# Performance work log

Measured on AMD Instinct MI355X. Metric: run time of the kernel, lower is better.

## Reference

```python
import jax, jax.numpy as jnp
import numpy as np

N = 50000   # nodes
E = 400000  # edges (before self-loops)
F = 128     # num_features
H = 8       # heads (layer 1)
C = 64      # hidden_channels
B = 64      # graphs in batch
K = 10      # num_classes
NEG_SLOPE = 0.2


def setup_inputs() -> dict:
    key = jax.random.key(0)
    ks = jax.random.split(key, 12)
    g = lambda k, shape, fan: jax.random.normal(k, shape, jnp.float32) / np.sqrt(fan).astype(np.float32)
    return {
        "x": jax.random.normal(ks[0], (N, F), jnp.float32),
        "edge_index": jax.random.randint(ks[1], (2, E), 0, N, jnp.int32),
        "batch": jnp.sort(jax.random.randint(ks[2], (N,), 0, B, jnp.int32)),
        "W1": g(ks[3], (F, H * C), F),
        "att_src1": g(ks[4], (H, C), C),
        "att_dst1": g(ks[5], (H, C), C),
        "b1": jnp.zeros((H * C,), jnp.float32),
        "W2": g(ks[6], (H * C, C), H * C),
        "att_src2": g(ks[7], (1, C), C),
        "att_dst2": g(ks[8], (1, C), C),
        "b2": jnp.zeros((C,), jnp.float32),
        "lin1_w": g(ks[9], (C, C), C),
        "lin1_b": jnp.zeros((C,), jnp.float32),
        "lin2_w": g(ks[10], (C, K), C),
        "lin2_b": jnp.zeros((K,), jnp.float32),
    }


def gat_conv(x, src, dst, W, att_src, att_dst, bias):
    """PyG GATConv (self-loops already appended to src/dst). x:[N,Fin] -> [N,H*C]."""
    heads, out_c = att_src.shape
    h = (x @ W).reshape(N, heads, out_c)                      # [N,H,C]
    a_s = jnp.einsum('nhc,hc->nh', h, att_src)                # [N,H]
    a_d = jnp.einsum('nhc,hc->nh', h, att_dst)
    e = jax.nn.leaky_relu(a_s[src] + a_d[dst], NEG_SLOPE)     # [E',H]
    # segment softmax over incoming edges of each destination node
    m = jax.ops.segment_max(e, dst, num_segments=N)
    e = jnp.exp(e - m[dst])
    denom = jax.ops.segment_sum(e, dst, num_segments=N)
    alpha = e / (denom[dst] + 1e-16)                          # [E',H]
    out = jax.ops.segment_sum(h[src] * alpha[:, :, None], dst, num_segments=N)  # [N,H,C]
    return out.reshape(N, heads * out_c) + bias


def reference(x, edge_index, batch, W1, att_src1, att_dst1, b1,
              W2, att_src2, att_dst2, b2, lin1_w, lin1_b, lin2_w, lin2_b):
    loops = jnp.arange(N, dtype=edge_index.dtype)
    src = jnp.concatenate([edge_index[0], loops])
    dst = jnp.concatenate([edge_index[1], loops])

    h = gat_conv(x, src, dst, W1, att_src1, att_dst1, b1)     # [N, H*C]
    h = jax.nn.elu(h)                                         # dropout inactive (eval)
    h = gat_conv(h, src, dst, W2, att_src2, att_dst2, b2)     # [N, C]
    h = jax.nn.elu(h)

    pooled = jax.ops.segment_sum(h, batch, num_segments=B)    # global_add_pool -> [B, C]
    z = jax.nn.elu(pooled @ lin1_w + lin1_b)
    logits = z @ lin2_w + lin2_b
    return jax.nn.log_softmax(logits, axis=-1)
```

## Files before the change

### kernel.cpp

```cpp
#include <hip/hip_runtime.h>
#include <hip/hip_bf16.h>

#define DEV static __device__ __forceinline__

constexpr int F1 = 128;
constexpr int H1 = 8;
constexpr int C  = 64;
constexpr int B  = 64;
constexpr int K  = 10;
constexpr float NEG = 0.2f;

typedef __attribute__((ext_vector_type(8))) short short8;
typedef __attribute__((ext_vector_type(4))) float floatx4;

DEV float b2f(__hip_bfloat16 x) { return __bfloat162float(x); }
DEV float elu1(float v) { return v > 0.f ? v : (__expf(v) - 1.f); }
DEV unsigned short f2bbits(float f) {
  __hip_bfloat16 b = __float2bfloat16(f);
  return *(unsigned short*)&b;
}
DEV float blo(unsigned u) { return __uint_as_float(u << 16); }
DEV float bhi(unsigned u) { return __uint_as_float(u & 0xffff0000u); }
DEV float bu(unsigned short u) { return __uint_as_float(((unsigned)u) << 16); }
DEV unsigned pack2(float lo, float hi) {
  return (unsigned)f2bbits(lo) | ((unsigned)f2bbits(hi) << 16);
}


DEV int detect_dev(const void* xraw, int* lds) {
  if (threadIdx.x == 0) {
    const __hip_bfloat16* xb = (const __hip_bfloat16*)xraw;
    int bad = 0;
    for (int i = 0; i < 128; ++i) {
      float v = b2f(xb[2 * i]);
      if (!(fabsf(v) < 1e4f)) bad++;
    }
    *lds = (bad < 13) ? 1 : 0;
  }
  __syncthreads();
  return *lds;
}

#define CVT(p, i) (isbf ? b2f(((const __hip_bfloat16*)(p))[i]) : ((const float*)(p))[i])

__global__ void fused_prep_kernel(const void* x_raw, const void* w1raw,
                                  const void* as1r, const void* ad1r, const void* b1r,
                                  const void* w2raw,
                                  const void* as2r, const void* ad2r, const void* b2r,
                                  const void* l1wr, const void* l1br,
                                  const void* l2wr, const void* l2br,
                                  unsigned short* __restrict__ xbf,
                                  unsigned short* __restrict__ w1frag,
                                  unsigned short* __restrict__ w2frag,
                                  float* __restrict__ wts,
                                  int* __restrict__ deg,
                                  float* __restrict__ pooled,
                                  int nX, int N) {
  __shared__ int fl;
  int isbf = detect_dev(x_raw, &fl);
  int gid = blockIdx.x * 256 + threadIdx.x;
  int stride = gridDim.x * 256;

  if (isbf) {
    const unsigned short* src = (const unsigned short*)x_raw;
    for (int i = gid; i < nX; i += stride) xbf[i] = src[i];
  } else {
    const float* src = (const float*)x_raw;
    for (int i = gid; i < nX; i += stride) xbf[i] = f2bbits(src[i]);
  }
  for (int i = gid; i < 512;  i += stride) wts[0    + i] = CVT(as1r, i);
  for (int i = gid; i < 512;  i += stride) wts[512  + i] = CVT(ad1r, i);
  for (int i = gid; i < 512;  i += stride) {
    int hp = i >> 7, l16 = (i >> 3) & 15, nt = i & 7;
    int c = hp * 128 + nt * 16 + l16;
    wts[1024 + i] = CVT(b1r, c);
  }
  for (int i = gid; i < 64;   i += stride) wts[1536 + i] = CVT(as2r, i);
  for (int i = gid; i < 64;   i += stride) wts[1600 + i] = CVT(ad2r, i);
  for (int i = gid; i < 64;   i += stride) wts[1664 + i] = CVT(b2r, i);
  for (int i = gid; i < 4096; i += stride) wts[1728 + i] = CVT(l1wr, i);
  for (int i = gid; i < 64;   i += stride) wts[5824 + i] = CVT(l1br, i);
  for (int i = gid; i < 640;  i += stride) wts[5888 + i] = CVT(l2wr, i);
  for (int i = gid; i < 10;   i += stride) wts[6528 + i] = CVT(l2br, i);
  for (int t = gid; t < 8192; t += stride) {
    int lane = t & 63, ks = (t >> 6) & 3, nt = t >> 8;
    for (int j = 0; j < 8; ++j) {
      int k = ks * 32 + (lane >> 4) * 8 + j;
      int n = nt * 16 + (lane & 15);
      w1frag[t * 8 + j] = f2bbits(CVT(w1raw, k * 512 + n));
    }
  }
  for (int t = gid; t < 4096; t += stride) {
    int lane = t & 63, nt = (t >> 6) & 3, ks = t >> 8;
    for (int j = 0; j < 8; ++j) {
      int p = ks * 32 + (lane >> 4) * 8 + j;
      int hp = p >> 7, pl16 = (p >> 3) & 15, pnt = p & 7;
      int k = hp * 128 + pnt * 16 + pl16;
      int n = nt * 16 + (lane & 15);
      w2frag[t * 8 + j] = f2bbits(CVT(w2raw, k * 64 + n));
    }
  }
  for (int i = gid; i < N; i += stride) deg[i] = 0;
  for (int i = gid; i < B * C; i += stride) pooled[i] = 0.f;
}

__global__ void deg_count_kernel(const int* __restrict__ ei, int E, int Etot,
                                 int* __restrict__ deg) {
  int e = blockIdx.x * blockDim.x + threadIdx.x;
  if (e >= Etot) return;
  int d = (e < E) ? ei[E + e] : e - E;
  atomicAdd(&deg[d], 1);
}

__global__ void scan_block_kernel(const int* __restrict__ deg,
                                  int* __restrict__ local,
                                  int* __restrict__ bsum, int N) {
  __shared__ int tmp[256];
  int t = threadIdx.x;
  int i = blockIdx.x * 256 + t;
  int v = (i < N) ? deg[i] : 0;
  tmp[t] = v;
  __syncthreads();
  for (int off = 1; off < 256; off <<= 1) {
    int u = (t >= off) ? tmp[t - off] : 0;
    __syncthreads();
    tmp[t] += u;
    __syncthreads();
  }
  if (i < N) local[i] = tmp[t] - v;
  if (t == 255) bsum[blockIdx.x] = tmp[255];
}

__global__ void scan_finish_kernel(const int* __restrict__ local,
                                   const int* __restrict__ bsum, int nb,
                                   int* __restrict__ rowptr,
                                   int* __restrict__ cursor, int N, int Etot) {
  __shared__ int tmp[256];
  __shared__ int offs;
  int t = threadIdx.x;
  int v0 = (t < nb) ? bsum[t] : 0;
  tmp[t] = v0;
  __syncthreads();
  for (int off = 1; off < 256; off <<= 1) {
    int u = (t >= off) ? tmp[t - off] : 0;
    __syncthreads();
    tmp[t] += u;
    __syncthreads();
  }
  if (t == (int)blockIdx.x) offs = tmp[t] - v0;
  __syncthreads();
  int i = blockIdx.x * 256 + t;
  if (i < N) {
    int r = local[i] + offs;
    rowptr[i] = r;
    cursor[i] = r;
  }
  if (i == 0) rowptr[N] = Etot;
}

__global__ __launch_bounds__(256) void gemm1_att_kernel(
    const unsigned short* __restrict__ xbf,
    const unsigned short* __restrict__ W1frag,
    const float* __restrict__ att_src,
    const float* __restrict__ att_dst,
    float* __restrict__ a_s, float* __restrict__ a_d,
    int N) {
  __shared__ __align__(16) unsigned short Xls[64 * 136];
  int t = threadIdx.x;
  int w = t >> 6, lane = t & 63;
  int quad = lane >> 4, l16 = lane & 15;
  int blkbase = blockIdx.x * 64;
  int rowbase = blkbase + w * 16;

  for (int idx = t; idx < 1024; idx += 256) {
    int row = idx >> 4, c = idx & 15;
    int rg = blkbase + row; if (rg >= N) rg = N - 1;
    *(uint4*)&Xls[row * 136 + c * 8] =
        *(const uint4*)(xbf + (size_t)rg * 128 + c * 8);
  }
  __syncthreads();

  short8 afr[4];
  {
    int rl = w * 16 + l16;
#pragma unroll
    for (int ks = 0; ks < 4; ++ks)
      afr[ks] = *(const short8*)&Xls[rl * 136 + ks * 32 + quad * 8];
  }

  for (int hp = 0; hp < 4; ++hp) {
    floatx4 acc[8] = {};
    const unsigned short* Bp = W1frag + (size_t)hp * 16384;
#pragma unroll
    for (int nt = 0; nt < 8; ++nt)
#pragma unroll
      for (int ks = 0; ks < 4; ++ks) {
        short8 b = *(const short8*)&Bp[((nt * 4 + ks) * 64 + lane) * 8];
        acc[nt] = __builtin_amdgcn_mfma_f32_16x16x32_bf16(afr[ks], b, acc[nt], 0, 0, 0);
      }

    float asw[8], adw[8];
#pragma unroll
    for (int nt = 0; nt < 8; ++nt) {
      asw[nt] = att_src[hp * 128 + nt * 16 + l16];
      adw[nt] = att_dst[hp * 128 + nt * 16 + l16];
    }
    float ps[2][4] = {}, pd[2][4] = {};
#pragma unroll
    for (int nt = 0; nt < 8; ++nt) {
      int hl = nt >> 2;
#pragma unroll
      for (int r = 0; r < 4; ++r) {
        ps[hl][r] += acc[nt][r] * asw[nt];
        pd[hl][r] += acc[nt][r] * adw[nt];
      }
    }
#pragma unroll
    for (int hl = 0; hl < 2; ++hl)
#pragma unroll
      for (int r = 0; r < 4; ++r) {
        float p = ps[hl][r], q = pd[hl][r];
#pragma unroll
        for (int off = 1; off < 16; off <<= 1) {
          p += __shfl_xor(p, off);
          q += __shfl_xor(q, off);
        }
        int row = rowbase + quad * 4 + r;
        if (l16 == 0 && row < N) {
          a_s[(size_t)row * 8 + hp * 2 + hl] = p;
          a_d[(size_t)row * 8 + hp * 2 + hl] = q;
        }
      }
  }
}

__global__ void fill_weight_kernel(const int* __restrict__ ei, int E, int Etot,
                                   const float* __restrict__ a_s,
                                   const float* __restrict__ a_d,
                                   int* __restrict__ cursor,
                                   int* __restrict__ col,
                                   float* __restrict__ wedge) {
  int e = blockIdx.x * 256 + threadIdx.x;
  if (e >= Etot) return;
  int s, d;
  if (e < E) { s = ei[e]; d = ei[E + e]; } else { s = d = e - E; }
  int pos = atomicAdd(&cursor[d], 1);
  col[pos] = s;
  float4 s0 = *(const float4*)(a_s + (size_t)s * 8);
  float4 s1 = *(const float4*)(a_s + (size_t)s * 8 + 4);
  float4 d0 = *(const float4*)(a_d + (size_t)d * 8);
  float4 d1 = *(const float4*)(a_d + (size_t)d * 8 + 4);
  float4 w0, w1;
  float v;
  v = s0.x + d0.x; v = v > 0.f ? v : NEG * v; w0.x = __expf(v);
  v = s0.y + d0.y; v = v > 0.f ? v : NEG * v; w0.y = __expf(v);
  v = s0.z + d0.z; v = v > 0.f ? v : NEG * v; w0.z = __expf(v);
  v = s0.w + d0.w; v = v > 0.f ? v : NEG * v; w0.w = __expf(v);
  v = s1.x + d1.x; v = v > 0.f ? v : NEG * v; w1.x = __expf(v);
  v = s1.y + d1.y; v = v > 0.f ? v : NEG * v; w1.y = __expf(v);
  v = s1.z + d1.z; v = v > 0.f ? v : NEG * v; w1.z = __expf(v);
  v = s1.w + d1.w; v = v > 0.f ? v : NEG * v; w1.w = __expf(v);
  *(float4*)(wedge + (size_t)pos * 8)     = w0;
  *(float4*)(wedge + (size_t)pos * 8 + 4) = w1;
}

__global__ __launch_bounds__(256) void aggx_gemm1_kernel(
    const unsigned short* __restrict__ xbf,
    const unsigned short* __restrict__ W1frag,
    const int* __restrict__ rowptr,
    const int* __restrict__ col,
    const float* __restrict__ wedge,
    const float* __restrict__ bias_perm,
    unsigned short* __restrict__ out1,
    int N) {
  __shared__ __align__(16) unsigned short Agg[8 * 16 * 136];
  int t = threadIdx.x, w = t >> 6, lane = t & 63;
  int dbase = blockIdx.x * 16;
  const unsigned* xd = (const unsigned*)xbf;
  unsigned* AggU = (unsigned*)Agg;

  for (int j = 0; j < 4; ++j) {
    int dloc = w * 4 + j;
    int d = dbase + dloc;
    int dd = d < N ? d : N - 1;
    int beg = rowptr[dd], end = rowptr[dd + 1];
    float acc[16] = {};
    float dn[8] = {};
#pragma unroll 4
    for (int i = beg; i < end; ++i) {
      int iu = __builtin_amdgcn_readfirstlane(i);
      int s = col[iu];
      unsigned xv = xd[(size_t)s * 64 + lane];
      float4 wa = *(const float4*)(wedge + (size_t)iu * 8);
      float4 wb = *(const float4*)(wedge + (size_t)iu * 8 + 4);
      float x0 = blo(xv), x1 = bhi(xv);
      acc[0]  += wa.x * x0; acc[1]  += wa.x * x1; dn[0] += wa.x;
      acc[2]  += wa.y * x0; acc[3]  += wa.y * x1; dn[1] += wa.y;
      acc[4]  += wa.z * x0; acc[5]  += wa.z * x1; dn[2] += wa.z;
      acc[6]  += wa.w * x0; acc[7]  += wa.w * x1; dn[3] += wa.w;
      acc[8]  += wb.x * x0; acc[9]  += wb.x * x1; dn[4] += wb.x;
      acc[10] += wb.y * x0; acc[11] += wb.y * x1; dn[5] += wb.y;
      acc[12] += wb.z * x0; acc[13] += wb.z * x1; dn[6] += wb.z;
      acc[14] += wb.w * x0; acc[15] += wb.w * x1; dn[7] += wb.w;
    }
#pragma unroll
    for (int h = 0; h < 8; ++h) {
      float inv = 1.f / (dn[h] + 1e-16f);
      AggU[(h * 16 + dloc) * 68 + lane] =
          pack2(acc[2 * h] * inv, acc[2 * h + 1] * inv);
    }
  }
  __syncthreads();

  int quad = lane >> 4, l16 = lane & 15;
  int hp = w;
  short8 afr[2][4];
#pragma unroll
  for (int hh = 0; hh < 2; ++hh) {
    int h = hp * 2 + hh;
#pragma unroll
    for (int ks = 0; ks < 4; ++ks)
      afr[hh][ks] = *(const short8*)&Agg[(h * 16 + l16) * 136 + ks * 32 + quad * 8];
  }
  floatx4 acc2[8] = {};
  const unsigned short* Bp = W1frag + (size_t)hp * 16384;
#pragma unroll
  for (int nt = 0; nt < 8; ++nt) {
    int hh = nt >> 2;
#pragma unroll
    for (int ks = 0; ks < 4; ++ks) {
      short8 b = *(const short8*)&Bp[((nt * 4 + ks) * 64 + lane) * 8];
      acc2[nt] = __builtin_amdgcn_mfma_f32_16x16x32_bf16(afr[hh][ks], b, acc2[nt], 0, 0, 0);
    }
  }
  float4 b0 = *(const float4*)&bias_perm[hp * 128 + l16 * 8];
  float4 b1 = *(const float4*)&bias_perm[hp * 128 + l16 * 8 + 4];
#pragma unroll
  for (int r = 0; r < 4; ++r) {
    int row = dbase + quad * 4 + r;
    if (row < N) {
      uint4 o;
      o.x = pack2(elu1(acc2[0][r] + b0.x), elu1(acc2[1][r] + b0.y));
      o.y = pack2(elu1(acc2[2][r] + b0.z), elu1(acc2[3][r] + b0.w));
      o.z = pack2(elu1(acc2[4][r] + b1.x), elu1(acc2[5][r] + b1.y));
      o.w = pack2(elu1(acc2[6][r] + b1.z), elu1(acc2[7][r] + b1.w));
      *(uint4*)&out1[(size_t)row * 512 + hp * 128 + l16 * 8] = o;
    }
  }
}

__global__ __launch_bounds__(256) void gemm2_mfma_kernel(
    const unsigned short* __restrict__ x2bf,
    const unsigned short* __restrict__ W2frag,
    const float* __restrict__ att_src,
    const float* __restrict__ att_dst,
    unsigned short* __restrict__ h2,
    float* __restrict__ a_s, float* __restrict__ a_d,
    int N) {
  int t = threadIdx.x;
  int w = t >> 6, lane = t & 63;
  int quad = lane >> 4, l16 = lane & 15;
  int rowbase = blockIdx.x * 64 + w * 16;

  floatx4 acc[4] = {};
  int r0 = rowbase + l16; if (r0 >= N) r0 = N - 1;
  const unsigned short* p0 = x2bf + (size_t)r0 * 512 + quad * 8;
#pragma unroll
  for (int ks = 0; ks < 16; ++ks) {
    short8 a0 = *(const short8*)(p0 + ks * 32);
#pragma unroll
    for (int nt = 0; nt < 4; ++nt) {
      short8 b = *(const short8*)&W2frag[((ks * 4 + nt) * 64 + lane) * 8];
      acc[nt] = __builtin_amdgcn_mfma_f32_16x16x32_bf16(a0, b, acc[nt], 0, 0, 0);
    }
  }

  float asw[4], adw[4];
#pragma unroll
  for (int nt = 0; nt < 4; ++nt) {
    asw[nt] = att_src[nt * 16 + l16];
    adw[nt] = att_dst[nt * 16 + l16];
  }
  float ps[4] = {}, pd[4] = {};
#pragma unroll
  for (int nt = 0; nt < 4; ++nt)
#pragma unroll
    for (int r = 0; r < 4; ++r) {
      float v = acc[nt][r];
      int row = rowbase + quad * 4 + r;
      if (row < N) h2[(size_t)row * 64 + nt * 16 + l16] = f2bbits(v);
      ps[r] += v * asw[nt];
      pd[r] += v * adw[nt];
    }
#pragma unroll
  for (int r = 0; r < 4; ++r) {
    float p = ps[r], q = pd[r];
#pragma unroll
    for (int off = 1; off < 16; off <<= 1) {
      p += __shfl_xor(p, off);
      q += __shfl_xor(q, off);
    }
    int row = rowbase + quad * 4 + r;
    if (l16 == 0 && row < N) {
      a_s[row] = p;
      a_d[row] = q;
    }
  }
}

__global__ void gat_agg1_kernel(const int* __restrict__ rowptr,
                                const int* __restrict__ col,
                                const float* __restrict__ a_s,
                                const float* __restrict__ a_d,
                                const unsigned short* __restrict__ hfeat,
                                const float* __restrict__ bias,
                                unsigned short* __restrict__ out, int N) {
  int wave = threadIdx.x >> 6, lane = threadIdx.x & 63;
  int d = blockIdx.x * 4 + wave;
  if (d >= N) return;
  int beg = rowptr[d], end = rowptr[d + 1];
  int qg = lane >> 4, l16 = lane & 15;
  float adv = a_d[d];
  const uint2* hfu = (const uint2*)hfeat;
  float acc[4] = {};
  float wsum = 0.f;
#pragma unroll 2
  for (int i = beg + qg; i < end; i += 4) {
    int s = col[i];
    float v = a_s[s] + adv;
    v = v > 0.f ? v : NEG * v;
    float wv = __expf(v);
    wsum += wv;
    uint2 u = hfu[(size_t)s * 16 + l16];
    acc[0] += wv * blo(u.x); acc[1] += wv * bhi(u.x);
    acc[2] += wv * blo(u.y); acc[3] += wv * bhi(u.y);
  }
#pragma unroll
  for (int off = 16; off <= 32; off <<= 1) {
#pragma unroll
    for (int j = 0; j < 4; ++j) acc[j] += __shfl_xor(acc[j], off);
    wsum += __shfl_xor(wsum, off);
  }
  float winv = 1.f / (wsum + 1e-16f);
  float4 bb = ((const float4*)bias)[l16];
  float r0 = elu1(acc[0] * winv + bb.x), r1 = elu1(acc[1] * winv + bb.y);
  float r2 = elu1(acc[2] * winv + bb.z), r3 = elu1(acc[3] * winv + bb.w);
  if (qg == 0) {
    uint2 o; o.x = pack2(r0, r1); o.y = pack2(r2, r3);
    ((uint2*)out)[(size_t)d * 16 + l16] = o;
  }
}

__global__ void pool_kernel(const unsigned short* __restrict__ out2,
                            const int* __restrict__ batch,
                            float* __restrict__ pooled, int N) {
  int wave = threadIdx.x >> 6, lane = threadIdx.x & 63;
  int seg = blockIdx.x * 4 + wave;
  int start = seg * 16;
  if (start >= N) return;
  int end = min(start + 16, N);
  int cur = batch[start];
  float acc = 0.f;
  for (int n = start; n < end; ++n) {
    int bn = batch[n];
    if (bn != cur) {
      unsafeAtomicAdd(&pooled[cur * 64 + lane], acc);
      acc = 0.f; cur = bn;
    }
    acc += bu(out2[(size_t)n * 64 + lane]);
  }
  unsafeAtomicAdd(&pooled[cur * 64 + lane], acc);
}

__global__ void head_kernel(const float* __restrict__ pooled,
                            const float* __restrict__ lin1_w,
                            const float* __restrict__ lin1_b,
                            const float* __restrict__ lin2_w,
                            const float* __restrict__ lin2_b,
                            const void* __restrict__ x_raw,
                            void* __restrict__ outv) {
  __shared__ float P[C];
  __shared__ float Zs[C];
  __shared__ float Ls[K];
  __shared__ float lse_s;
  __shared__ int fl;
  int isbf = detect_dev(x_raw, &fl);
  int g = blockIdx.x, t = threadIdx.x;
  P[t] = pooled[g * C + t];
  __syncthreads();
  float acc = lin1_b[t];
  for (int k = 0; k < C; ++k) acc += P[k] * lin1_w[k * C + t];
  Zs[t] = elu1(acc);
  __syncthreads();
  if (t < K) {
    float a = lin2_b[t];
    for (int k = 0; k < C; ++k) a += Zs[k] * lin2_w[k * K + t];
    Ls[t] = a;
  }
  __syncthreads();
  if (t == 0) {
    float mx = -1e30f;
    for (int c = 0; c < K; ++c) mx = fmaxf(mx, Ls[c]);
    float s = 0.f;
    for (int c = 0; c < K; ++c) s += __expf(Ls[c] - mx);
    lse_s = mx + __logf(s);
  }
  __syncthreads();
  if (t < K) {
    float val = Ls[t] - lse_s;
    if (isbf) ((__hip_bfloat16*)outv)[g * K + t] = __float2bfloat16(val);
    else      ((float*)outv)[g * K + t] = val;
  }
}

extern "C" void kernel_launch(void* const* d_in, const int* in_sizes, int n_in,
                              void* d_out, int out_size, void* d_ws, size_t ws_size,
                              hipStream_t stream) {
  const void* x_raw = d_in[0];
  const int*  ei    = (const int*)d_in[1];
  const int*  batch = (const int*)d_in[2];

  const int N    = in_sizes[2];
  const int E    = in_sizes[1] / 2;
  const int Etot = E + N;
  const int nb   = (N + 255) / 256;

  float* ws   = (float*)d_ws;
  size_t off  = 0;

  float* wts = ws + off; off += 6544;
  float* as1w = wts + 0;
  float* ad1w = wts + 512;
  float* b1w  = wts + 1024;
  float* as2w = wts + 1536;
  float* ad2w = wts + 1600;
  float* b2w  = wts + 1664;
  float* l1w  = wts + 1728;
  float* l1b  = wts + 5824;
  float* l2w  = wts + 5888;
  float* l2b  = wts + 6528;

  unsigned short* xbf    = (unsigned short*)(ws + off); off += (size_t)N * 64;
  unsigned short* w1frag = (unsigned short*)(ws + off); off += 32768;
  unsigned short* w2frag = (unsigned short*)(ws + off); off += 16384;
  float* wedge           = ws + off;                    off += (size_t)Etot * 8;
  unsigned short* out1bf = (unsigned short*)(ws + off); off += (size_t)N * 256;
  unsigned short* h2bf   = (unsigned short*)(ws + off); off += (size_t)N * 32;
  unsigned short* out2bf = (unsigned short*)(ws + off); off += (size_t)N * 32;
  float* as1  = ws + off; off += (size_t)N * H1;
  float* ad1  = ws + off; off += (size_t)N * H1;
  float* as2  = ws + off; off += (size_t)N;
  float* ad2  = ws + off; off += (size_t)N;
  float* pooled = ws + off; off += (size_t)B * C;

  int* ibase  = (int*)(ws + off);
  int* deg    = ibase;                 ibase += N;
  int* cursor = ibase;                 ibase += N;
  int* rowptr = ibase;                 ibase += N + 1;
  int* locals = ibase;                 ibase += N;
  int* bsum   = ibase;                 ibase += 256;
  int* col    = ibase;                 ibase += Etot;

  fused_prep_kernel<<<1024, 256, 0, stream>>>(
      x_raw, d_in[3], d_in[4], d_in[5], d_in[6], d_in[7], d_in[8], d_in[9],
      d_in[10], d_in[11], d_in[12], d_in[13], d_in[14],
      xbf, w1frag, w2frag, wts, deg, pooled, in_sizes[0], N);

  deg_count_kernel<<<(Etot + 255) / 256, 256, 0, stream>>>(ei, E, Etot, deg);
  scan_block_kernel<<<nb, 256, 0, stream>>>(deg, locals, bsum, N);
  scan_finish_kernel<<<nb, 256, 0, stream>>>(locals, bsum, nb, rowptr, cursor, N, Etot);

  gemm1_att_kernel<<<(N + 63) / 64, 256, 0, stream>>>(xbf, w1frag, as1w, ad1w,
                                                      as1, ad1, N);

  fill_weight_kernel<<<(Etot + 255) / 256, 256, 0, stream>>>(
      ei, E, Etot, as1, ad1, cursor, col, wedge);

  aggx_gemm1_kernel<<<(N + 15) / 16, 256, 0, stream>>>(
      xbf, w1frag, rowptr, col, wedge, b1w, out1bf, N);

  gemm2_mfma_kernel<<<(N + 63) / 64, 256, 0, stream>>>(out1bf, w2frag, as2w, ad2w,
                                                       h2bf, as2, ad2, N);
  gat_agg1_kernel<<<(N + 3) / 4, 256, 0, stream>>>(rowptr, col, as2, ad2, h2bf, b2w, out2bf, N);

  pool_kernel<<<(N + 63) / 64, 256, 0, stream>>>(out2bf, batch, pooled, N);
  head_kernel<<<B, 64, 0, stream>>>(pooled, l1w, l1b, l2w, l2b, x_raw, (void*)d_out);
}
```

Baseline: 332.0 us.

## Fold attention vectors into W1 and restructure layer-1 aggregation blocks

Precomputes W1·att_src and W1·att_dst into a small 128x16 bf16 MFMA fragment, so layer-1 attention scalars come from a single K=128 MFMA per row tile instead of a full 128x512 GEMM followed by reductions. The aggregation+GEMM kernel moves to 512 threads with 8 destinations per block, one warp per destination, and uses packed v_pk_fma/v_pk_add with SGPR-broadcast weights plus an approximate reciprocal refined by one Newton step. This removes a large redundant GEMM. The trade-offs are a different rounding order for the attention scalars (the folded vector is rounded to bf16) and half-filled 16-row MFMA tiles in the aggregation kernel.

Result: faster. 303.8 us (-8.5%).

```diff
diff --git a/kernel.cpp b/kernel.cpp
--- a/kernel.cpp
+++ b/kernel.cpp
@@ -12,6 +12,7 @@
 
 typedef __attribute__((ext_vector_type(8))) short short8;
 typedef __attribute__((ext_vector_type(4))) float floatx4;
+typedef __attribute__((ext_vector_type(2))) float floatx2;
 
 DEV float b2f(__hip_bfloat16 x) { return __bfloat162float(x); }
 DEV float elu1(float v) { return v > 0.f ? v : (__expf(v) - 1.f); }
@@ -24,6 +25,16 @@
 DEV float bu(unsigned short u) { return __uint_as_float(((unsigned)u) << 16); }
 DEV unsigned pack2(float lo, float hi) {
   return (unsigned)f2bbits(lo) | ((unsigned)f2bbits(hi) << 16);
+}
+DEV float rcp_nr(float x) {
+  float r = __builtin_amdgcn_rcpf(x);
+  return r * (2.f - x * r);
+}
+DEV void pk_fma(floatx2& acc, floatx2 x, floatx2 w) {
+  asm("v_pk_fma_f32 %0, %1, %2, %0" : "+v"(acc) : "v"(x), "s"(w));
+}
+DEV void pk_add(floatx2& acc, floatx2 w) {
+  asm("v_pk_add_f32 %0, %0, %1" : "+v"(acc) : "s"(w));
 }
 
 
@@ -52,6 +63,7 @@
                                   unsigned short* __restrict__ xbf,
                                   unsigned short* __restrict__ w1frag,
                                   unsigned short* __restrict__ w2frag,
+                                  unsigned short* __restrict__ vfrag,
                                   float* __restrict__ wts,
                                   int* __restrict__ deg,
                                   float* __restrict__ pooled,
@@ -68,8 +80,6 @@
     const float* src = (const float*)x_raw;
     for (int i = gid; i < nX; i += stride) xbf[i] = f2bbits(src[i]);
   }
-  for (int i = gid; i < 512;  i += stride) wts[0    + i] = CVT(as1r, i);
-  for (int i = gid; i < 512;  i += stride) wts[512  + i] = CVT(ad1r, i);
   for (int i = gid; i < 512;  i += stride) {
     int hp = i >> 7, l16 = (i >> 3) & 15, nt = i & 7;
     int c = hp * 128 + nt * 16 + l16;
@@ -100,6 +110,21 @@
       w2frag[t * 8 + j] = f2bbits(CVT(w2raw, k * 64 + n));
     }
   }
+  for (int t = gid; t < 2048; t += stride) {
+    int j = t & 7, lane = (t >> 3) & 63, ks = t >> 9;
+    int k = ks * 32 + (lane >> 4) * 8 + j;
+    int n = lane & 15;
+    int hh = (n < 8) ? n : (n - 8);
+    float s = 0.f;
+    if (n < 8) {
+      for (int c = 0; c < 64; ++c)
+        s += CVT(w1raw, k * 512 + hh * 64 + c) * CVT(as1r, hh * 64 + c);
+    } else {
+      for (int c = 0; c < 64; ++c)
+        s += CVT(w1raw, k * 512 + hh * 64 + c) * CVT(ad1r, hh * 64 + c);
+    }
+    vfrag[(ks * 64 + lane) * 8 + j] = f2bbits(s);
+  }
   for (int i = gid; i < N; i += stride) deg[i] = 0;
   for (int i = gid; i < B * C; i += stride) pooled[i] = 0.f;
 }
@@ -158,79 +183,31 @@
   if (i == 0) rowptr[N] = Etot;
 }
 
-__global__ __launch_bounds__(256) void gemm1_att_kernel(
+__global__ __launch_bounds__(256) void att_scalars_kernel(
     const unsigned short* __restrict__ xbf,
-    const unsigned short* __restrict__ W1frag,
-    const float* __restrict__ att_src,
-    const float* __restrict__ att_dst,
+    const unsigned short* __restrict__ vfrag,
     float* __restrict__ a_s, float* __restrict__ a_d,
     int N) {
-  __shared__ __align__(16) unsigned short Xls[64 * 136];
-  int t = threadIdx.x;
-  int w = t >> 6, lane = t & 63;
+  int t = threadIdx.x, w = t >> 6, lane = t & 63;
   int quad = lane >> 4, l16 = lane & 15;
-  int blkbase = blockIdx.x * 64;
-  int rowbase = blkbase + w * 16;
-
-  for (int idx = t; idx < 1024; idx += 256) {
-    int row = idx >> 4, c = idx & 15;
-    int rg = blkbase + row; if (rg >= N) rg = N - 1;
-    *(uint4*)&Xls[row * 136 + c * 8] =
-        *(const uint4*)(xbf + (size_t)rg * 128 + c * 8);
-  }
-  __syncthreads();
-
-  short8 afr[4];
-  {
-    int rl = w * 16 + l16;
-#pragma unroll
-    for (int ks = 0; ks < 4; ++ks)
-      afr[ks] = *(const short8*)&Xls[rl * 136 + ks * 32 + quad * 8];
-  }
-
-  for (int hp = 0; hp < 4; ++hp) {
-    floatx4 acc[8] = {};
-    const unsigned short* Bp = W1frag + (size_t)hp * 16384;
-#pragma unroll
-    for (int nt = 0; nt < 8; ++nt)
-#pragma unroll
-      for (int ks = 0; ks < 4; ++ks) {
-        short8 b = *(const short8*)&Bp[((nt * 4 + ks) * 64 + lane) * 8];
-        acc[nt] = __builtin_amdgcn_mfma_f32_16x16x32_bf16(afr[ks], b, acc[nt], 0, 0, 0);
-      }
-
-    float asw[8], adw[8];
-#pragma unroll
-    for (int nt = 0; nt < 8; ++nt) {
-      asw[nt] = att_src[hp * 128 + nt * 16 + l16];
-      adw[nt] = att_dst[hp * 128 + nt * 16 + l16];
-    }
-    float ps[2][4] = {}, pd[2][4] = {};
-#pragma unroll
-    for (int nt = 0; nt < 8; ++nt) {
-      int hl = nt >> 2;
-#pragma unroll
-      for (int r = 0; r < 4; ++r) {
-        ps[hl][r] += acc[nt][r] * asw[nt];
-        pd[hl][r] += acc[nt][r] * adw[nt];
-      }
-    }
-#pragma unroll
-    for (int hl = 0; hl < 2; ++hl)
-#pragma unroll
-      for (int r = 0; r < 4; ++r) {
-        float p = ps[hl][r], q = pd[hl][r];
-#pragma unroll
-        for (int off = 1; off < 16; off <<= 1) {
-          p += __shfl_xor(p, off);
-          q += __shfl_xor(q, off);
-        }
-        int row = rowbase + quad * 4 + r;
-        if (l16 == 0 && row < N) {
-          a_s[(size_t)row * 8 + hp * 2 + hl] = p;
-          a_d[(size_t)row * 8 + hp * 2 + hl] = q;
-        }
-      }
+  int row0 = blockIdx.x * 64 + w * 16;
+
+  floatx4 acc = {};
+  int rl = row0 + l16; if (rl >= N) rl = N - 1;
+  const unsigned short* xp = xbf + (size_t)rl * 128 + quad * 8;
+#pragma unroll
+  for (int ks = 0; ks < 4; ++ks) {
+    short8 a = *(const short8*)(xp + ks * 32);
+    short8 b = *(const short8*)&vfrag[(ks * 64 + lane) * 8];
+    acc = __builtin_amdgcn_mfma_f32_16x16x32_bf16(a, b, acc, 0, 0, 0);
+  }
+#pragma unroll
+  for (int r = 0; r < 4; ++r) {
+    int row = row0 + quad * 4 + r;
+    if (row < N) {
+      if (l16 < 8) a_s[(size_t)row * 8 + l16] = acc[r];
+      else         a_d[(size_t)row * 8 + (l16 - 8)] = acc[r];
+    }
   }
 }
 
@@ -264,7 +241,7 @@
   *(float4*)(wedge + (size_t)pos * 8 + 4) = w1;
 }
 
-__global__ __launch_bounds__(256) void aggx_gemm1_kernel(
+__global__ __launch_bounds__(512, 8) void aggx_gemm1_kernel(
     const unsigned short* __restrict__ xbf,
     const unsigned short* __restrict__ W1frag,
     const int* __restrict__ rowptr,
@@ -273,78 +250,76 @@
     const float* __restrict__ bias_perm,
     unsigned short* __restrict__ out1,
     int N) {
-  __shared__ __align__(16) unsigned short Agg[8 * 16 * 136];
+  __shared__ __align__(16) unsigned short Agg[8 * 8 * 144];
   int t = threadIdx.x, w = t >> 6, lane = t & 63;
-  int dbase = blockIdx.x * 16;
+  int dbase = blockIdx.x * 8;
   const unsigned* xd = (const unsigned*)xbf;
   unsigned* AggU = (unsigned*)Agg;
 
-  for (int j = 0; j < 4; ++j) {
-    int dloc = w * 4 + j;
-    int d = dbase + dloc;
+  {
+    int d = dbase + w;
     int dd = d < N ? d : N - 1;
     int beg = rowptr[dd], end = rowptr[dd + 1];
-    float acc[16] = {};
-    float dn[8] = {};
-#pragma unroll 4
+    floatx2 acc[8] = {};
+    floatx2 dn01 = {}, dn23 = {}, dn45 = {}, dn67 = {};
+#pragma unroll 2
     for (int i = beg; i < end; ++i) {
       int iu = __builtin_amdgcn_readfirstlane(i);
       int s = col[iu];
-      unsigned xv = xd[(size_t)s * 64 + lane];
-      float4 wa = *(const float4*)(wedge + (size_t)iu * 8);
-      float4 wb = *(const float4*)(wedge + (size_t)iu * 8 + 4);
-      float x0 = blo(xv), x1 = bhi(xv);
-      acc[0]  += wa.x * x0; acc[1]  += wa.x * x1; dn[0] += wa.x;
-      acc[2]  += wa.y * x0; acc[3]  += wa.y * x1; dn[1] += wa.y;
-      acc[4]  += wa.z * x0; acc[5]  += wa.z * x1; dn[2] += wa.z;
-      acc[6]  += wa.w * x0; acc[7]  += wa.w * x1; dn[3] += wa.w;
-      acc[8]  += wb.x * x0; acc[9]  += wb.x * x1; dn[4] += wb.x;
-      acc[10] += wb.y * x0; acc[11] += wb.y * x1; dn[5] += wb.y;
-      acc[12] += wb.z * x0; acc[13] += wb.z * x1; dn[6] += wb.z;
-      acc[14] += wb.w * x0; acc[15] += wb.w * x1; dn[7] += wb.w;
-    }
-#pragma unroll
-    for (int h = 0; h < 8; ++h) {
-      float inv = 1.f / (dn[h] + 1e-16f);
-      AggU[(h * 16 + dloc) * 68 + lane] =
-          pack2(acc[2 * h] * inv, acc[2 * h + 1] * inv);
-    }
-  }
-  __syncthreads();
-
-  int quad = lane >> 4, l16 = lane & 15;
-  int hp = w;
-  short8 afr[2][4];
-#pragma unroll
-  for (int hh = 0; hh < 2; ++hh) {
-    int h = hp * 2 + hh;
-#pragma unroll
-    for (int ks = 0; ks < 4; ++ks)
-      afr[hh][ks] = *(const short8*)&Agg[(h * 16 + l16) * 136 + ks * 32 + quad * 8];
-  }
-  floatx4 acc2[8] = {};
-  const unsigned short* Bp = W1frag + (size_t)hp * 16384;
-#pragma unroll
-  for (int nt = 0; nt < 8; ++nt) {
-    int hh = nt >> 2;
+      unsigned xv = xd[((size_t)s << 6) + lane];
+      const float* wp = wedge + (size_t)iu * 8;
+      float w0 = wp[0], w1 = wp[1], w2 = wp[2], w3 = wp[3];
+      float w4 = wp[4], w5 = wp[5], w6 = wp[6], w7 = wp[7];
+      floatx2 p01 = {w0, w1}, p23 = {w2, w3}, p45 = {w4, w5}, p67 = {w6, w7};
+      pk_add(dn01, p01); pk_add(dn23, p23);
+      pk_add(dn45, p45); pk_add(dn67, p67);
+      floatx2 xp; xp.x = blo(xv); xp.y = bhi(xv);
+      floatx2 b0 = {w0, w0}, b1 = {w1, w1}, b2 = {w2, w2}, b3 = {w3, w3};
+      floatx2 b4 = {w4, w4}, b5 = {w5, w5}, b6 = {w6, w6}, b7 = {w7, w7};
+      pk_fma(acc[0], xp, b0); pk_fma(acc[1], xp, b1);
+      pk_fma(acc[2], xp, b2); pk_fma(acc[3], xp, b3);
+      pk_fma(acc[4], xp, b4); pk_fma(acc[5], xp, b5);
+      pk_fma(acc[6], xp, b6); pk_fma(acc[7], xp, b7);
+    }
+    float inv[8];
+    inv[0] = rcp_nr(dn01.x + 1e-16f); inv[1] = rcp_nr(dn01.y + 1e-16f);
+    inv[2] = rcp_nr(dn23.x + 1e-16f); inv[3] = rcp_nr(dn23.y + 1e-16f);
+    inv[4] = rcp_nr(dn45.x + 1e-16f); inv[5] = rcp_nr(dn45.y + 1e-16f);
+    inv[6] = rcp_nr(dn67.x + 1e-16f); inv[7] = rcp_nr(dn67.y + 1e-16f);
+#pragma unroll
+    for (int h = 0; h < 8; ++h)
+      AggU[(h * 8 + w) * 72 + lane] =
+          pack2(acc[h].x * inv[h], acc[h].y * inv[h]);
+  }
+  __syncthreads();
+
+  {
+    int quad = lane >> 4, l16 = lane & 15;
+    int hp = w >> 1, q = w & 1;
+    int h = hp * 2 + q;
+    floatx4 acc2[4] = {};
+    const unsigned short* Bp = W1frag + (size_t)hp * 16384;
 #pragma unroll
     for (int ks = 0; ks < 4; ++ks) {
-      short8 b = *(const short8*)&Bp[((nt * 4 + ks) * 64 + lane) * 8];
-      acc2[nt] = __builtin_amdgcn_mfma_f32_16x16x32_bf16(afr[hh][ks], b, acc2[nt], 0, 0, 0);
-    }
-  }
-  float4 b0 = *(const float4*)&bias_perm[hp * 128 + l16 * 8];
-  float4 b1 = *(const float4*)&bias_perm[hp * 128 + l16 * 8 + 4];
-#pragma unroll
-  for (int r = 0; r < 4; ++r) {
-    int row = dbase + quad * 4 + r;
-    if (row < N) {
-      uint4 o;
-      o.x = pack2(elu1(acc2[0][r] + b0.x), elu1(acc2[1][r] + b0.y));
-      o.y = pack2(elu1(acc2[2][r] + b0.z), elu1(acc2[3][r] + b0.w));
-      o.z = pack2(elu1(acc2[4][r] + b1.x), elu1(acc2[5][r] + b1.y));
-      o.w = pack2(elu1(acc2[6][r] + b1.z), elu1(acc2[7][r] + b1.w));
-      *(uint4*)&out1[(size_t)row * 512 + hp * 128 + l16 * 8] = o;
+      short8 a = *(const short8*)&Agg[(h * 8 + (l16 & 7)) * 144 + ks * 32 + quad * 8];
+#pragma unroll
+      for (int j = 0; j < 4; ++j) {
+        int nt = q * 4 + j;
+        short8 b = *(const short8*)&Bp[((nt * 4 + ks) * 64 + lane) * 8];
+        acc2[j] = __builtin_amdgcn_mfma_f32_16x16x32_bf16(a, b, acc2[j], 0, 0, 0);
+      }
+    }
+    float4 bq = *(const float4*)&bias_perm[hp * 128 + l16 * 8 + q * 4];
+#pragma unroll
+    for (int r = 0; r < 4; ++r) {
+      int dl = quad * 4 + r;
+      int row = dbase + dl;
+      if (dl < 8 && row < N) {
+        uint2 o;
+        o.x = pack2(elu1(acc2[0][r] + bq.x), elu1(acc2[1][r] + bq.y));
+        o.y = pack2(elu1(acc2[2][r] + bq.z), elu1(acc2[3][r] + bq.w));
+        *(uint2*)&out1[(size_t)row * 512 + hp * 128 + l16 * 8 + q * 4] = o;
+      }
     }
   }
 }
@@ -529,8 +504,6 @@
   size_t off  = 0;
 
   float* wts = ws + off; off += 6544;
-  float* as1w = wts + 0;
-  float* ad1w = wts + 512;
   float* b1w  = wts + 1024;
   float* as2w = wts + 1536;
   float* ad2w = wts + 1600;
@@ -543,6 +516,7 @@
   unsigned short* xbf    = (unsigned short*)(ws + off); off += (size_t)N * 64;
   unsigned short* w1frag = (unsigned short*)(ws + off); off += 32768;
   unsigned short* w2frag = (unsigned short*)(ws + off); off += 16384;
+  unsigned short* vfrag  = (unsigned short*)(ws + off); off += 1024;
   float* wedge           = ws + off;                    off += (size_t)Etot * 8;
   unsigned short* out1bf = (unsigned short*)(ws + off); off += (size_t)N * 256;
   unsigned short* h2bf   = (unsigned short*)(ws + off); off += (size_t)N * 32;
@@ -564,19 +538,18 @@
   fused_prep_kernel<<<1024, 256, 0, stream>>>(
       x_raw, d_in[3], d_in[4], d_in[5], d_in[6], d_in[7], d_in[8], d_in[9],
       d_in[10], d_in[11], d_in[12], d_in[13], d_in[14],
-      xbf, w1frag, w2frag, wts, deg, pooled, in_sizes[0], N);
+      xbf, w1frag, w2frag, vfrag, wts, deg, pooled, in_sizes[0], N);
 
   deg_count_kernel<<<(Etot + 255) / 256, 256, 0, stream>>>(ei, E, Etot, deg);
   scan_block_kernel<<<nb, 256, 0, stream>>>(deg, locals, bsum, N);
   scan_finish_kernel<<<nb, 256, 0, stream>>>(locals, bsum, nb, rowptr, cursor, N, Etot);
 
-  gemm1_att_kernel<<<(N + 63) / 64, 256, 0, stream>>>(xbf, w1frag, as1w, ad1w,
-                                                      as1, ad1, N);
+  att_scalars_kernel<<<(N + 63) / 64, 256, 0, stream>>>(xbf, vfrag, as1, ad1, N);
 
   fill_weight_kernel<<<(Etot + 255) / 256, 256, 0, stream>>>(
       ei, E, Etot, as1, ad1, cursor, col, wedge);
 
-  aggx_gemm1_kernel<<<(N + 15) / 16, 256, 0, stream>>>(
+  aggx_gemm1_kernel<<<(N + 7) / 8, 512, 0, stream>>>(
       xbf, w1frag, rowptr, col, wedge, b1w, out1bf, N);
 
   gemm2_mfma_kernel<<<(N + 63) / 64, 256, 0, stream>>>(out1bf, w2frag, as2w, ad2w,
```
